# Optimization experiments

Hardware: AMD Instinct MI355X
Metric: run time of the kernel (lower is better)

Reference implementation:

```python
import jax, jax.numpy as jnp
import numpy as np

NEG = -1e30   # safe -inf surrogate
EPS = 1e-7    # keras.backend.epsilon() used by ctc_batch_cost


def setup_inputs() -> dict:
    key = jax.random.key(0)
    k1, k2 = jax.random.split(key)
    B, T, C, L = 512, 512, 256, 64
    u = jax.random.uniform(k1, (B, T, C), dtype=jnp.float32, minval=1e-3, maxval=1.0)
    y_pred = u / jnp.sum(u, axis=-1, keepdims=True)  # softmax-like probabilities
    y_true = jax.random.randint(k2, (B, L), 0, C - 1)  # labels in [0, C-2]; blank = C-1
    return {"y_true": y_true, "y_pred": y_pred}


def ctc_loss(y_true, y_pred):
    # Faithful to K.ctc_batch_cost with label_length = L, input_length = T for all samples.
    B, T, C = y_pred.shape
    L = y_true.shape[1]
    S = 2 * L + 1            # extended label length (blanks interleaved)
    blank = C - 1            # TF CTC convention: blank is last class
    labels = y_true.astype(jnp.int32)

    # extended labels: [blank, l1, blank, l2, ..., lL, blank]
    ext = jnp.full((B, S), blank, dtype=jnp.int32).at[:, 1::2].set(labels)
    prev2 = jnp.concatenate([jnp.full((B, 2), blank, jnp.int32), ext[:, :-2]], axis=1)
    # transition s-2 -> s allowed only for non-blank states with ext[s] != ext[s-2]
    skip = (ext != blank) & (ext != prev2)

    logp = jnp.log(y_pred + EPS)                                   # [B,T,C]
    idx = jnp.broadcast_to(ext[:, None, :], (B, T, S))
    lp_ext = jnp.take_along_axis(logp, idx, axis=2)                # [B,T,S]

    # alpha at t=0: only states 0 (blank) and 1 (first label) reachable
    alpha0 = jnp.full((B, S), NEG, dtype=logp.dtype)
    alpha0 = alpha0.at[:, 0].set(lp_ext[:, 0, 0]).at[:, 1].set(lp_ext[:, 0, 1])

    def step(alpha, lp_t):
        a1 = jnp.concatenate([jnp.full((B, 1), NEG, alpha.dtype), alpha[:, :-1]], axis=1)
        a2 = jnp.concatenate([jnp.full((B, 2), NEG, alpha.dtype), alpha[:, :-2]], axis=1)
        m = jnp.logaddexp(jnp.logaddexp(alpha, a1), jnp.where(skip, a2, NEG))
        return m + lp_t, None

    lp_seq = jnp.transpose(lp_ext, (1, 0, 2))[1:]                  # [T-1,B,S]
    alphaT, _ = jax.lax.scan(step, alpha0, lp_seq)

    # total log-likelihood ends in last blank or last label
    loss = -jnp.logaddexp(alphaT[:, S - 1], alphaT[:, S - 2])      # [B]
    return loss[:, None]                                           # [B,1] like ctc_batch_cost


def reference(y_true, y_pred):
    return ctc_loss(y_true, y_pred)
```

## Files before the change

kernel.cpp:

```cpp
#include <hip/hip_runtime.h>


#define NEGF (-1e30f)
#define EPSF (1e-7f)

constexpr int T_  = 512;
constexpr int C_  = 256;
constexpr int L_  = 64;
constexpr int TCH = 16;
constexpr int NCH = T_ / TCH;

__device__ __forceinline__ float lae2(float a, float b) {
    float m = fmaxf(a, b);
    float d = fminf(a, b) - m;
    return m + __logf(1.0f + __expf(d));
}

__device__ __forceinline__ float wave_shr1(float x) {
    int r = __builtin_amdgcn_update_dpp(0, __float_as_int(x),
                                        0x138 ,
                                        0xF, 0xF, true );
    return __int_as_float(r);
}

typedef const __attribute__((address_space(1))) void GV;
typedef __attribute__((address_space(3))) void LV;

__global__ __launch_bounds__(256, 1)
void ctc_kernel(const int* __restrict__ y_true,
                const float* __restrict__ y_pred,
                float* __restrict__ out) {
    __shared__ float rawb[2][TCH * C_];
    __shared__ float lpLs[2][TCH][64];
    __shared__ float lpBs[2][TCH];

    const int b     = blockIdx.x;
    const int tid   = threadIdx.x;
    const int lane  = tid & 63;
    const int wid   = tid >> 6;
    const int blank = C_ - 1;

    const float* __restrict__ row = y_pred + (size_t)b * T_ * C_;

    if (wid != 0) {
        const int e1 = y_true[b * L_ + lane];

        auto stage = [&](int c, int buf) {
            const float* s = row + (size_t)c * TCH * C_ + lane * 4;
            for (int r = wid - 1; r < TCH; r += 3) {
                __builtin_amdgcn_global_load_lds((GV*)(s + r * C_),
                                                 (LV*)(&rawb[buf][r * C_]),
                                                 16, 0, 0);
            }
        };
        auto produce = [&](int buf) {
            for (int r = wid - 1; r < TCH; r += 3) {
                float pe = rawb[buf][r * C_ + e1];
                float pb = rawb[buf][r * C_ + blank];
                lpLs[buf][r][lane] = __logf(pe + EPSF);
                if (lane == 0) lpBs[buf][r] = __logf(pb + EPSF);
            }
        };

        stage(0, 0);
        stage(1, 1);
        __builtin_amdgcn_s_waitcnt(0x0F70);
        produce(0);
        __syncthreads();

        for (int c = 0; c < NCH; ++c) {
            if (c + 2 < NCH) stage(c + 2, c & 1);
            if (c + 1 < NCH) produce((c + 1) & 1);
            __syncthreads();
        }
        return;
    }

    const int e1    = y_true[b * L_ + lane];
    const int eprev = (lane == 0) ? blank : y_true[b * L_ + lane - 1];
    const bool skip1 = (e1 != blank) && (e1 != eprev);

    float a0 = NEGF, a1 = NEGF, a2 = NEGF;

    __syncthreads();

    for (int c = 0; c < NCH; ++c) {
        const int cb = c & 1;

        float l0[TCH], l1[TCH];
#pragma unroll
        for (int j = 0; j < TCH; ++j) {
            l1[j] = lpLs[cb][j][lane];
            l0[j] = lpBs[cb][j];
        }

#pragma unroll
        for (int j = 0; j < TCH; ++j) {
            const float lp0 = l0[j];
            const float lp1 = l1[j];
            if (c == 0 && j == 0) {
                a0 = (lane == 0) ? lp0 : NEGF;
                a1 = (lane == 0) ? lp1 : NEGF;
                a2 = NEGF;
            } else {
                float pa1 = wave_shr1(a1);
                if (lane == 0) pa1 = NEGF;

                const float na0 = lae2(a0, pa1) + lp0;

                const float c3 = skip1 ? pa1 : NEGF;
                const float m  = fmaxf(fmaxf(a1, a0), c3);
                const float s  = __expf(a1 - m) + __expf(a0 - m) + __expf(c3 - m);
                const float na1 = m + __logf(s) + lp1;

                const float na2 = lae2(a2, a1) + lp0;

                a0 = na0; a1 = na1; a2 = na2;
            }
        }
        __syncthreads();
    }

    if (lane == 63) {
        out[b] = -lae2(a1, a2);
    }
}

extern "C" void kernel_launch(void* const* d_in, const int* in_sizes, int n_in,
                              void* d_out, int out_size, void* d_ws, size_t ws_size,
                              hipStream_t stream) {
    const int*   y_true = (const int*)d_in[0];
    const float* y_pred = (const float*)d_in[1];
    float*       out    = (float*)d_out;

    const int B = in_sizes[0] / L_;
    ctc_kernel<<<dim3(B), dim3(256), 0, stream>>>(y_true, y_pred, out);
}
```

Measured before the change: 366.8 us.

## Run CTC alpha recursion in linear space with periodic power-of-two renormalization

Replaces the log-space logaddexp recursion with a probability-space recursion using plain multiply-adds, renormalising every four steps by a power-of-two scale taken from a wave-wide max, and tracking the exponent separately. The producer side drops the LDS staging buffer: two waves load rows into registers and pick out the label and blank probabilities with shuffles and readlane, and the block shrinks from four waves to three. This removes most exp and log work from the serial critical path. The trade-off is possible underflow between renormalisations and different numerics from the log-space reference.

```diff
diff --git a/kernel.cpp b/kernel.cpp
--- a/kernel.cpp
+++ b/kernel.cpp
@@ -1,38 +1,43 @@
 #include <hip/hip_runtime.h>
 
 
-#define NEGF (-1e30f)
 #define EPSF (1e-7f)
 
-constexpr int T_  = 512;
-constexpr int C_  = 256;
-constexpr int L_  = 64;
-constexpr int TCH = 16;
-constexpr int NCH = T_ / TCH;
-
-__device__ __forceinline__ float lae2(float a, float b) {
-    float m = fmaxf(a, b);
-    float d = fminf(a, b) - m;
-    return m + __logf(1.0f + __expf(d));
-}
+constexpr int T_   = 512;
+constexpr int C_   = 256;
+constexpr int L_   = 64;
+constexpr int TCH  = 16;
+constexpr int NCH  = T_ / TCH;
+constexpr int RPW  = TCH / 2;
 
 __device__ __forceinline__ float wave_shr1(float x) {
     int r = __builtin_amdgcn_update_dpp(0, __float_as_int(x),
-                                        0x138 ,
-                                        0xF, 0xF, true );
+                                        0x138 , 0xF, 0xF, true);
     return __int_as_float(r);
 }
 
-typedef const __attribute__((address_space(1))) void GV;
-typedef __attribute__((address_space(3))) void LV;
+template <int CTRL>
+__device__ __forceinline__ float dppmax(float x) {
+    int t = __builtin_amdgcn_update_dpp(0, __float_as_int(x), CTRL, 0xF, 0xF, true);
+    return fmaxf(x, __int_as_float(t));
+}
 
-__global__ __launch_bounds__(256, 1)
+__device__ __forceinline__ float wave_max_u(float x) {
+    x = dppmax<0x111>(x);
+    x = dppmax<0x112>(x);
+    x = dppmax<0x114>(x);
+    x = dppmax<0x118>(x);
+    x = dppmax<0x142>(x);
+    x = dppmax<0x143>(x);
+    return __int_as_float(__builtin_amdgcn_readlane(__float_as_int(x), 63));
+}
+
+__global__ __launch_bounds__(192, 1)
 void ctc_kernel(const int* __restrict__ y_true,
                 const float* __restrict__ y_pred,
                 float* __restrict__ out) {
-    __shared__ float rawb[2][TCH * C_];
-    __shared__ float lpLs[2][TCH][64];
-    __shared__ float lpBs[2][TCH];
+    __shared__ float pLs[2][TCH][64];
+    __shared__ float pBs[2][TCH];
 
     const int b     = blockIdx.x;
     const int tid   = threadIdx.x;
@@ -41,88 +46,113 @@
     const int blank = C_ - 1;
 
     const float* __restrict__ row = y_pred + (size_t)b * T_ * C_;
+    const int q = y_true[b * L_ + lane];
 
     if (wid != 0) {
-        const int e1 = y_true[b * L_ + lane];
+        const int  srcl  = q >> 2;
+        const int  rbase = (wid - 1) * RPW;
+        const float4* src = (const float4*)row + lane;
 
-        auto stage = [&](int c, int buf) {
-            const float* s = row + (size_t)c * TCH * C_ + lane * 4;
-            for (int r = wid - 1; r < TCH; r += 3) {
-                __builtin_amdgcn_global_load_lds((GV*)(s + r * C_),
-                                                 (LV*)(&rawb[buf][r * C_]),
-                                                 16, 0, 0);
-            }
+        float4 A[RPW], B[RPW];
+        auto loadC = [&](int c, float4* buf) {
+#pragma unroll
+            for (int r = 0; r < RPW; ++r)
+                buf[r] = src[(size_t)(c * TCH + rbase + r) * (C_ / 4)];
         };
-        auto produce = [&](int buf) {
-            for (int r = wid - 1; r < TCH; r += 3) {
-                float pe = rawb[buf][r * C_ + e1];
-                float pb = rawb[buf][r * C_ + blank];
-                lpLs[buf][r][lane] = __logf(pe + EPSF);
-                if (lane == 0) lpBs[buf][r] = __logf(pb + EPSF);
+        auto prod = [&](int slot, const float4* buf) {
+#pragma unroll
+            for (int r = 0; r < RPW; ++r) {
+                const float4 f = buf[r];
+                const float vx = __shfl(f.x, srcl, 64);
+                const float vy = __shfl(f.y, srcl, 64);
+                const float vz = __shfl(f.z, srcl, 64);
+                const float vw = __shfl(f.w, srcl, 64);
+                const float t0 = (q & 2) ? vz : vx;
+                const float t1 = (q & 2) ? vw : vy;
+                const float pe = (q & 1) ? t1 : t0;
+                pLs[slot][rbase + r][lane] = pe + EPSF;
+                const float pbv = __int_as_float(
+                    __builtin_amdgcn_readlane(__float_as_int(f.w), 63));
+                if (lane == 0) pBs[slot][rbase + r] = pbv + EPSF;
             }
         };
 
-        stage(0, 0);
-        stage(1, 1);
-        __builtin_amdgcn_s_waitcnt(0x0F70);
-        produce(0);
-        __syncthreads();
+        loadC(0, A); loadC(1, B);
+        prod(0, A);
+        loadC(2, A);
+        __builtin_amdgcn_s_waitcnt(0xC07F);
+        __builtin_amdgcn_s_barrier();
 
-        for (int c = 0; c < NCH; ++c) {
-            if (c + 2 < NCH) stage(c + 2, c & 1);
-            if (c + 1 < NCH) produce((c + 1) & 1);
-            __syncthreads();
+        for (int c = 0; c + 1 < NCH; c += 2) {
+            prod(1, B);
+            if (c + 3 < NCH) loadC(c + 3, B);
+            __builtin_amdgcn_s_waitcnt(0xC07F);
+            __builtin_amdgcn_s_barrier();
+            if (c + 2 < NCH) {
+                prod(0, A);
+                if (c + 4 < NCH) loadC(c + 4, A);
+                __builtin_amdgcn_s_waitcnt(0xC07F);
+                __builtin_amdgcn_s_barrier();
+            }
         }
         return;
     }
 
-    const int e1    = y_true[b * L_ + lane];
-    const int eprev = (lane == 0) ? blank : y_true[b * L_ + lane - 1];
-    const bool skip1 = (e1 != blank) && (e1 != eprev);
+    const int  pidx  = (lane == 0) ? 0 : (lane - 1);
+    const int  qp    = y_true[b * L_ + pidx];
+    const bool skip1 = (q != blank) && (lane != 0) && (q != qp);
 
-    float a0 = NEGF, a1 = NEGF, a2 = NEGF;
+    float a0 = 0.0f, a1 = 0.0f, a2 = 0.0f;
+    int   kexp = 0;
+
+    auto renorm = [&]() {
+        float m = wave_max_u(fmaxf(fmaxf(a0, a1), a2));
+        m = fmaxf(m, 1e-35f);
+        const int   e  = (__float_as_int(m) >> 23) - 127;
+        const float sc = __int_as_float((127 - e) << 23);
+        a0 *= sc; a1 *= sc; a2 *= sc; kexp += e;
+    };
+    auto step = [&](float p0, float p1) {
+        const float pa1 = wave_shr1(a1);
+        const float na0 = (a0 + pa1) * p0;
+        const float c3  = skip1 ? pa1 : 0.0f;
+        const float na1 = (a1 + a0 + c3) * p1;
+        const float na2 = (a2 + a1) * p0;
+        a0 = na0; a1 = na1; a2 = na2;
+    };
 
     __syncthreads();
-
-    for (int c = 0; c < NCH; ++c) {
-        const int cb = c & 1;
-
-        float l0[TCH], l1[TCH];
+    {
+        float pl[TCH], pb[TCH];
+#pragma unroll
+        for (int j = 0; j < TCH; ++j) { pl[j] = pLs[0][j][lane]; pb[j] = pBs[0][j]; }
+        a0 = (lane == 0) ? pb[0] : 0.0f;
+        a1 = (lane == 0) ? pl[0] : 0.0f;
+        a2 = 0.0f;
+#pragma unroll
+        for (int j = 1; j < TCH; ++j) {
+            step(pb[j], pl[j]);
+            if ((j & 3) == 3) renorm();
+        }
+    }
+    auto consume = [&](int slot) {
+        float pl[TCH], pb[TCH];
+#pragma unroll
+        for (int j = 0; j < TCH; ++j) { pl[j] = pLs[slot][j][lane]; pb[j] = pBs[slot][j]; }
 #pragma unroll
         for (int j = 0; j < TCH; ++j) {
-            l1[j] = lpLs[cb][j][lane];
-            l0[j] = lpBs[cb][j];
+            step(pb[j], pl[j]);
+            if ((j & 3) == 3) renorm();
         }
-
-#pragma unroll
-        for (int j = 0; j < TCH; ++j) {
-            const float lp0 = l0[j];
-            const float lp1 = l1[j];
-            if (c == 0 && j == 0) {
-                a0 = (lane == 0) ? lp0 : NEGF;
-                a1 = (lane == 0) ? lp1 : NEGF;
-                a2 = NEGF;
-            } else {
-                float pa1 = wave_shr1(a1);
-                if (lane == 0) pa1 = NEGF;
-
-                const float na0 = lae2(a0, pa1) + lp0;
-
-                const float c3 = skip1 ? pa1 : NEGF;
-                const float m  = fmaxf(fmaxf(a1, a0), c3);
-                const float s  = __expf(a1 - m) + __expf(a0 - m) + __expf(c3 - m);
-                const float na1 = m + __logf(s) + lp1;
-
-                const float na2 = lae2(a2, a1) + lp0;
-
-                a0 = na0; a1 = na1; a2 = na2;
-            }
-        }
-        __syncthreads();
+    };
+    __syncthreads(); consume(1);
+    for (int c = 2; c < NCH; c += 2) {
+        __syncthreads(); consume(0);
+        __syncthreads(); consume(1);
     }
 
     if (lane == 63) {
-        out[b] = -lae2(a1, a2);
+        out[b] = -(__logf(a1 + a2) + (float)kexp * 0.69314718055994531f);
     }
 }
 
@@ -134,5 +164,5 @@
     float*       out    = (float*)d_out;
 
     const int B = in_sizes[0] / L_;
-    ctc_kernel<<<dim3(B), dim3(256), 0, stream>>>(y_true, y_pred, out);
+    ctc_kernel<<<dim3(B), dim3(192), 0, stream>>>(y_true, y_pred, out);
 }
```

After: 360.0 us. No clear change (-1.9%).

## Replace LDS-staged raw rows with register loads and wave-shuffle gather

Applied to the files above, without the earlier changes.

Producer waves now load y_pred rows straight into registers as float4 and pull the label probability out with cross-lane shuffles, instead of copying whole rows into LDS through global_load_lds. This removes the large raw LDS buffer, which lets more blocks fit per CU. The block grows to 8 waves (7 producers), the time chunk doubles to 32, and the register double-buffering uses explicit waitcnt and barriers. The risks are higher register pressure from the prefetch buffers and the cost of four shuffles per row.

```diff
diff --git a/kernel.cpp b/kernel.cpp
--- a/kernel.cpp
+++ b/kernel.cpp
@@ -7,8 +7,10 @@
 constexpr int T_  = 512;
 constexpr int C_  = 256;
 constexpr int L_  = 64;
-constexpr int TCH = 16;
+constexpr int TCH = 32;
 constexpr int NCH = T_ / TCH;
+constexpr int NPW = 7;
+constexpr int NRW = 5;
 
 __device__ __forceinline__ float lae2(float a, float b) {
     float m = fmaxf(a, b);
@@ -18,19 +20,14 @@
 
 __device__ __forceinline__ float wave_shr1(float x) {
     int r = __builtin_amdgcn_update_dpp(0, __float_as_int(x),
-                                        0x138 ,
-                                        0xF, 0xF, true );
+                                        0x138 , 0xF, 0xF, true);
     return __int_as_float(r);
 }
 
-typedef const __attribute__((address_space(1))) void GV;
-typedef __attribute__((address_space(3))) void LV;
-
-__global__ __launch_bounds__(256, 1)
+__global__ __launch_bounds__(512, 4)
 void ctc_kernel(const int* __restrict__ y_true,
                 const float* __restrict__ y_pred,
                 float* __restrict__ out) {
-    __shared__ float rawb[2][TCH * C_];
     __shared__ float lpLs[2][TCH][64];
     __shared__ float lpBs[2][TCH];
 
@@ -41,84 +38,105 @@
     const int blank = C_ - 1;
 
     const float* __restrict__ row = y_pred + (size_t)b * T_ * C_;
+    const int q = y_true[b * L_ + lane];
 
     if (wid != 0) {
-        const int e1 = y_true[b * L_ + lane];
+        const int w    = wid - 1;
+        const int srcl = q >> 2;
+        const float4* src = (const float4*)row + lane;
 
-        auto stage = [&](int c, int buf) {
-            const float* s = row + (size_t)c * TCH * C_ + lane * 4;
-            for (int r = wid - 1; r < TCH; r += 3) {
-                __builtin_amdgcn_global_load_lds((GV*)(s + r * C_),
-                                                 (LV*)(&rawb[buf][r * C_]),
-                                                 16, 0, 0);
+        float4 A[NRW], B[NRW];
+        auto loadC = [&](int c, float4* buf) {
+#pragma unroll
+            for (int i = 0; i < NRW; ++i) {
+                const int r = w + NPW * i;
+                if (r < TCH)
+                    buf[i] = src[(size_t)(c * TCH + r) * (C_ / 4)];
             }
         };
-        auto produce = [&](int buf) {
-            for (int r = wid - 1; r < TCH; r += 3) {
-                float pe = rawb[buf][r * C_ + e1];
-                float pb = rawb[buf][r * C_ + blank];
-                lpLs[buf][r][lane] = __logf(pe + EPSF);
-                if (lane == 0) lpBs[buf][r] = __logf(pb + EPSF);
+        auto produce = [&](int slot, const float4* buf) {
+#pragma unroll
+            for (int i = 0; i < NRW; ++i) {
+                const int r = w + NPW * i;
+                if (r < TCH) {
+                    const float4 f = buf[i];
+                    const float vx = __shfl(f.x, srcl, 64);
+                    const float vy = __shfl(f.y, srcl, 64);
+                    const float vz = __shfl(f.z, srcl, 64);
+                    const float vw = __shfl(f.w, srcl, 64);
+                    const float t0 = (q & 2) ? vz : vx;
+                    const float t1 = (q & 2) ? vw : vy;
+                    const float pe = (q & 1) ? t1 : t0;
+                    lpLs[slot][r][lane] = __logf(pe + EPSF);
+                    const float pb = __int_as_float(
+                        __builtin_amdgcn_readlane(__float_as_int(f.w), 63));
+                    const float lb = __logf(pb + EPSF);
+                    if (lane == 0) lpBs[slot][r] = lb;
+                }
             }
         };
 
-        stage(0, 0);
-        stage(1, 1);
-        __builtin_amdgcn_s_waitcnt(0x0F70);
-        produce(0);
-        __syncthreads();
-
-        for (int c = 0; c < NCH; ++c) {
-            if (c + 2 < NCH) stage(c + 2, c & 1);
-            if (c + 1 < NCH) produce((c + 1) & 1);
-            __syncthreads();
+        loadC(0, A); loadC(1, B);
+        produce(0, A); loadC(2, A);
+        __builtin_amdgcn_s_waitcnt(0xC07F);
+        __builtin_amdgcn_s_barrier();
+        for (int cc = 1; cc + 1 < NCH; cc += 2) {
+            produce(1, B);
+            if (cc + 2 < NCH) loadC(cc + 2, B);
+            __builtin_amdgcn_s_waitcnt(0xC07F);
+            __builtin_amdgcn_s_barrier();
+            produce(0, A);
+            if (cc + 3 < NCH) loadC(cc + 3, A);
+            __builtin_amdgcn_s_waitcnt(0xC07F);
+            __builtin_amdgcn_s_barrier();
         }
+        produce(1, B);
+        __builtin_amdgcn_s_waitcnt(0xC07F);
+        __builtin_amdgcn_s_barrier();
         return;
     }
 
-    const int e1    = y_true[b * L_ + lane];
-    const int eprev = (lane == 0) ? blank : y_true[b * L_ + lane - 1];
-    const bool skip1 = (e1 != blank) && (e1 != eprev);
+    const int  qp    = (lane == 0) ? blank : y_true[b * L_ + lane - 1];
+    const bool skip1 = (q != blank) && (q != qp);
 
     float a0 = NEGF, a1 = NEGF, a2 = NEGF;
 
+    auto step = [&](float lp0, float lp1) {
+        float pa1 = wave_shr1(a1);
+        if (lane == 0) pa1 = NEGF;
+        const float na0 = lae2(a0, pa1) + lp0;
+        const float c3  = skip1 ? pa1 : NEGF;
+        const float m   = fmaxf(fmaxf(a1, a0), c3);
+        const float s   = __expf(a1 - m) + __expf(a0 - m) + __expf(c3 - m);
+        const float na1 = m + __logf(s) + lp1;
+        const float na2 = lae2(a2, a1) + lp0;
+        a0 = na0; a1 = na1; a2 = na2;
+    };
+    auto half = [&](int slot, int jbase, bool init) {
+        float l1[16], l0[16];
+#pragma unroll
+        for (int j = 0; j < 16; ++j) {
+            l1[j] = lpLs[slot][jbase + j][lane];
+            l0[j] = lpBs[slot][jbase + j];
+        }
+        int j0 = 0;
+        if (init) {
+            a0 = (lane == 0) ? l0[0] : NEGF;
+            a1 = (lane == 0) ? l1[0] : NEGF;
+            a2 = NEGF;
+            j0 = 1;
+        }
+#pragma unroll
+        for (int j = 0; j < 16; ++j)
+            if (j >= j0) step(l0[j], l1[j]);
+    };
+
     __syncthreads();
-
-    for (int c = 0; c < NCH; ++c) {
-        const int cb = c & 1;
-
-        float l0[TCH], l1[TCH];
-#pragma unroll
-        for (int j = 0; j < TCH; ++j) {
-            l1[j] = lpLs[cb][j][lane];
-            l0[j] = lpBs[cb][j];
-        }
-
-#pragma unroll
-        for (int j = 0; j < TCH; ++j) {
-            const float lp0 = l0[j];
-            const float lp1 = l1[j];
-            if (c == 0 && j == 0) {
-                a0 = (lane == 0) ? lp0 : NEGF;
-                a1 = (lane == 0) ? lp1 : NEGF;
-                a2 = NEGF;
-            } else {
-                float pa1 = wave_shr1(a1);
-                if (lane == 0) pa1 = NEGF;
-
-                const float na0 = lae2(a0, pa1) + lp0;
-
-                const float c3 = skip1 ? pa1 : NEGF;
-                const float m  = fmaxf(fmaxf(a1, a0), c3);
-                const float s  = __expf(a1 - m) + __expf(a0 - m) + __expf(c3 - m);
-                const float na1 = m + __logf(s) + lp1;
-
-                const float na2 = lae2(a2, a1) + lp0;
-
-                a0 = na0; a1 = na1; a2 = na2;
-            }
-        }
+    half(0, 0, true); half(0, 16, false);
+    for (int c = 1; c < NCH; ++c) {
         __syncthreads();
+        const int slot = c & 1;
+        half(slot, 0, false); half(slot, 16, false);
     }
 
     if (lane == 63) {
@@ -134,5 +152,5 @@
     float*       out    = (float*)d_out;
 
     const int B = in_sizes[0] / L_;
-    ctc_kernel<<<dim3(B), dim3(256), 0, stream>>>(y_true, y_pred, out);
+    ctc_kernel<<<dim3(B), dim3(512), 0, stream>>>(y_true, y_pred, out);
 }
```

Measured after the change: 384.2 us. 1.05x slower.
